# Performance work log

Hardware: AMD Instinct MI355X
Metric: run time of the kernel (lower is better)

## Reference

```python
import jax, jax.numpy as jnp
import numpy as np

D_HID = 512          # RAECell output dim (nn.Linear(1024, 512))
DEPTH = 16           # internal levels -> 2**16 leaves, 131071 nodes


def _levels(left, right, leaf, root):
    """Group internal nodes by depth via host-side BFS (tree topology is static)."""
    levels = []
    frontier = [int(root)]
    while frontier:
        internal = [n for n in frontier if not leaf[n]]
        if internal:
            levels.append(np.asarray(internal, dtype=np.int32))
        frontier = [c for n in internal for c in (int(left[n]), int(right[n]))]
    return levels


def setup_inputs() -> dict:
    key = jax.random.key(0)
    n_leaves = 2 ** DEPTH
    n_nodes = 2 * n_leaves - 1
    first_leaf = n_leaves - 1
    idx = np.arange(n_nodes)
    # complete binary tree in heap layout
    left = np.where(idx < first_leaf, 2 * idx + 1, 0).astype(np.int64)
    right = np.where(idx < first_leaf, 2 * idx + 2, 0).astype(np.int64)
    is_leaf = (idx >= first_leaf).astype(np.int64)
    k1, k2, k3 = jax.random.split(key, 3)
    inp = jax.random.normal(k1, (n_nodes, D_HID), jnp.float32)
    W = jax.random.normal(k2, (D_HID, 2 * D_HID), jnp.float32) * (1.0 / np.sqrt(2 * D_HID))
    b = jax.random.normal(k3, (D_HID,), jnp.float32) * 0.01
    return {
        "left": jnp.asarray(left),
        "right": jnp.asarray(right),
        "is_leaf": jnp.asarray(is_leaf),
        "inp": inp,
        "root": 0,
        "W": W,
        "b": b,
    }


def reference(left, right, is_leaf, inp, root, W, b):
    # Tree indices are static -> pull to host once and batch the recursion
    # level-by-level (replaces the Python recursion + per-node tiny kernels
    # of the original with log2(N) batched concat+GEMM+tanh steps).
    l = np.asarray(left)
    r = np.asarray(right)
    leaf = np.asarray(is_leaf).astype(bool)
    levels = _levels(l, r, leaf, root)
    H = inp  # [n_nodes, 512]; leaf rows are the inputs, internal rows get overwritten bottom-up
    for lvl in reversed(levels):
        a = H[l[lvl]]              # [m, 512] left children
        c = H[r[lvl]]              # [m, 512] right children
        x = jnp.concatenate([a, c], axis=1)          # [m, 1024] == torch.cat((a, b))
        H = H.at[jnp.asarray(lvl)].set(jnp.tanh(x @ W.T + b))
    return H[int(root)]
```

## Files before the change

### kernel.cpp

```cpp
#include <hip/hip_runtime.h>
#include <hip/hip_fp16.h>

typedef _Float16 half8 __attribute__((ext_vector_type(8)));
typedef float f32x4 __attribute__((ext_vector_type(4)));

#define KDIM 1024
#define NDIM 512

#define GLOAD_LDS16(g, l) __builtin_amdgcn_global_load_lds(                 \
    (const __attribute__((address_space(1))) void*)(g),                     \
    (__attribute__((address_space(3))) void*)(l), 16, 0, 0)

__global__ __launch_bounds__(256, 2)
void rae_level_gemm_h(const _Float16* __restrict__ X, const _Float16* __restrict__ Wh,
                      const float* __restrict__ bias, _Float16* __restrict__ Yh)
{
    __shared__ _Float16 Xs[128 * 64];
    __shared__ _Float16 Ws[128 * 64];

    const int tid  = threadIdx.x;
    const int lane = tid & 63;
    const int wave = tid >> 6;
    const int wm = wave >> 1;
    const int wn = wave & 1;
    const int lrow = lane & 15;
    const int lq   = lane >> 4;

    const int brow = blockIdx.x * 128;
    const int bcol = blockIdx.y * 128;

    const int sr = tid >> 3;
    const int su = (((tid & 7) ^ (sr & 7)) << 3);

    const _Float16* xbase = X  + (size_t)(brow + sr) * KDIM + su;
    const _Float16* wbase = Wh + (size_t)(bcol + sr) * KDIM + su;

    f32x4 acc[4][4] = {};

    for (int k0 = 0; k0 < KDIM; k0 += 64) {
        __syncthreads();
        GLOAD_LDS16(xbase + k0,             Xs + tid * 8);
        GLOAD_LDS16(xbase + k0 + 32 * KDIM, Xs + tid * 8 + 2048);
        GLOAD_LDS16(xbase + k0 + 64 * KDIM, Xs + tid * 8 + 4096);
        GLOAD_LDS16(xbase + k0 + 96 * KDIM, Xs + tid * 8 + 6144);
        GLOAD_LDS16(wbase + k0,             Ws + tid * 8);
        GLOAD_LDS16(wbase + k0 + 32 * KDIM, Ws + tid * 8 + 2048);
        GLOAD_LDS16(wbase + k0 + 64 * KDIM, Ws + tid * 8 + 4096);
        GLOAD_LDS16(wbase + k0 + 96 * KDIM, Ws + tid * 8 + 6144);
        __syncthreads();

        #pragma unroll
        for (int ks = 0; ks < 2; ++ks) {
            half8 af[4], bf[4];
            #pragma unroll
            for (int i = 0; i < 4; ++i) {
                const int R = wm * 64 + i * 16 + lrow;
                const int phys = (ks * 4 + lq) ^ (R & 7);
                af[i] = *(const half8*)&Xs[R * 64 + phys * 8];
            }
            #pragma unroll
            for (int j = 0; j < 4; ++j) {
                const int R = wn * 64 + j * 16 + lrow;
                const int phys = (ks * 4 + lq) ^ (R & 7);
                bf[j] = *(const half8*)&Ws[R * 64 + phys * 8];
            }
            #pragma unroll
            for (int i = 0; i < 4; ++i)
                #pragma unroll
                for (int j = 0; j < 4; ++j)
                    acc[i][j] = __builtin_amdgcn_mfma_f32_16x16x32_f16(af[i], bf[j], acc[i][j], 0, 0, 0);
        }
    }

    #pragma unroll
    for (int j = 0; j < 4; ++j) {
        const int col = bcol + wn * 64 + j * 16 + lrow;
        const float bv = bias[col];
        #pragma unroll
        for (int i = 0; i < 4; ++i) {
            const int rbase = brow + wm * 64 + i * 16 + lq * 4;
            #pragma unroll
            for (int r = 0; r < 4; ++r)
                Yh[(size_t)(rbase + r) * NDIM + col] = (_Float16)tanhf(acc[i][j][r] + bv);
        }
    }
}

__global__ __launch_bounds__(256, 2)
void rae_level15_f32(const float* __restrict__ Xf, const _Float16* __restrict__ Wh,
                     const float* __restrict__ bias, _Float16* __restrict__ Yh)
{
    __shared__ _Float16 Xs[128 * 64];
    __shared__ _Float16 Ws[128 * 64];

    const int tid  = threadIdx.x;
    const int lane = tid & 63;
    const int wave = tid >> 6;
    const int wm = wave >> 1;
    const int wn = wave & 1;
    const int lrow = lane & 15;
    const int lq   = lane >> 4;

    const int brow = blockIdx.x * 128;
    const int bcol = blockIdx.y * 128;

    const int sr = tid >> 3;
    const int su = (((tid & 7) ^ (sr & 7)) << 3);

    const float*    xbase = Xf + (size_t)(brow + sr) * KDIM + su;
    const _Float16* wbase = Wh + (size_t)(bcol + sr) * KDIM + su;

    f32x4 acc[4][4] = {};

    for (int k0 = 0; k0 < KDIM; k0 += 64) {
        __syncthreads();
        GLOAD_LDS16(wbase + k0,             Ws + tid * 8);
        GLOAD_LDS16(wbase + k0 + 32 * KDIM, Ws + tid * 8 + 2048);
        GLOAD_LDS16(wbase + k0 + 64 * KDIM, Ws + tid * 8 + 4096);
        GLOAD_LDS16(wbase + k0 + 96 * KDIM, Ws + tid * 8 + 6144);
        #pragma unroll
        for (int c = 0; c < 4; ++c) {
            const float4* g = (const float4*)(xbase + k0 + (size_t)c * 32 * KDIM);
            const float4 aa = g[0];
            const float4 bb = g[1];
            half8 h;
            h[0] = (_Float16)aa.x; h[1] = (_Float16)aa.y;
            h[2] = (_Float16)aa.z; h[3] = (_Float16)aa.w;
            h[4] = (_Float16)bb.x; h[5] = (_Float16)bb.y;
            h[6] = (_Float16)bb.z; h[7] = (_Float16)bb.w;
            *(half8*)(Xs + tid * 8 + c * 2048) = h;
        }
        __syncthreads();

        #pragma unroll
        for (int ks = 0; ks < 2; ++ks) {
            half8 af[4], bf[4];
            #pragma unroll
            for (int i = 0; i < 4; ++i) {
                const int R = wm * 64 + i * 16 + lrow;
                const int phys = (ks * 4 + lq) ^ (R & 7);
                af[i] = *(const half8*)&Xs[R * 64 + phys * 8];
            }
            #pragma unroll
            for (int j = 0; j < 4; ++j) {
                const int R = wn * 64 + j * 16 + lrow;
                const int phys = (ks * 4 + lq) ^ (R & 7);
                bf[j] = *(const half8*)&Ws[R * 64 + phys * 8];
            }
            #pragma unroll
            for (int i = 0; i < 4; ++i)
                #pragma unroll
                for (int j = 0; j < 4; ++j)
                    acc[i][j] = __builtin_amdgcn_mfma_f32_16x16x32_f16(af[i], bf[j], acc[i][j], 0, 0, 0);
        }
    }

    #pragma unroll
    for (int j = 0; j < 4; ++j) {
        const int col = bcol + wn * 64 + j * 16 + lrow;
        const float bv = bias[col];
        #pragma unroll
        for (int i = 0; i < 4; ++i) {
            const int rbase = brow + wm * 64 + i * 16 + lq * 4;
            #pragma unroll
            for (int r = 0; r < 4; ++r)
                Yh[(size_t)(rbase + r) * NDIM + col] = (_Float16)tanhf(acc[i][j][r] + bv);
        }
    }
}

__device__ __forceinline__ void grid_barrier(unsigned* bar, unsigned nb)
{
    __syncthreads();
    if (threadIdx.x == 0) {
        __threadfence();
        unsigned* cnt = bar;
        unsigned* gen = bar + 32;
        unsigned g = __hip_atomic_load(gen, __ATOMIC_RELAXED, __HIP_MEMORY_SCOPE_AGENT);
        if (__hip_atomic_fetch_add(cnt, 1u, __ATOMIC_ACQ_REL, __HIP_MEMORY_SCOPE_AGENT) == nb - 1u) {
            __hip_atomic_store(cnt, 0u, __ATOMIC_RELAXED, __HIP_MEMORY_SCOPE_AGENT);
            __hip_atomic_store(gen, g + 1u, __ATOMIC_RELEASE, __HIP_MEMORY_SCOPE_AGENT);
        } else {
            while (__hip_atomic_load(gen, __ATOMIC_RELAXED, __HIP_MEMORY_SCOPE_AGENT) == g) {}
        }
        __threadfence();
    }
    __syncthreads();
}

#define TWLD 1032

template<int NF>
__device__ __forceinline__ void tail_level(
    int d, const _Float16* __restrict__ Hh, float* __restrict__ out,
    const float* __restrict__ bias, const _Float16* Ws,
    int col0, int gw, int lrow, int lq, _Float16* __restrict__ Y)
{
    const int m = 1 << d;
    const _Float16* X = Hh + ((size_t)(2 << d) - 1) * NDIM;
    const int rbase0 = gw * (NF * 16);
    if (rbase0 >= m) return;

    f32x4 acc[NF][2] = {};

    #pragma unroll
    for (int ks = 0; ks < 32; ++ks) {
        half8 af[NF], bf[2];
        #pragma unroll
        for (int i = 0; i < NF; ++i)
            af[i] = *(const half8*)(X + (size_t)(rbase0 + i * 16 + lrow) * KDIM + ks * 32 + lq * 8);
        #pragma unroll
        for (int j = 0; j < 2; ++j)
            bf[j] = *(const half8*)(Ws + (j * 16 + lrow) * TWLD + ks * 32 + lq * 8);
        #pragma unroll
        for (int i = 0; i < NF; ++i)
            #pragma unroll
            for (int j = 0; j < 2; ++j)
                acc[i][j] = __builtin_amdgcn_mfma_f32_16x16x32_f16(af[i], bf[j], acc[i][j], 0, 0, 0);
    }

    #pragma unroll
    for (int j = 0; j < 2; ++j) {
        const int col = col0 + j * 16 + lrow;
        const float bv = bias[col];
        #pragma unroll
        for (int i = 0; i < NF; ++i) {
            #pragma unroll
            for (int r = 0; r < 4; ++r) {
                const int row = rbase0 + i * 16 + lq * 4 + r;
                if (row < m) {
                    const float v = tanhf(acc[i][j][r] + bv);
                    if (d == 0) out[col] = v;
                    else Y[(size_t)row * NDIM + col] = (_Float16)v;
                }
            }
        }
    }
}

__global__ __launch_bounds__(512, 2)
void rae_tail(const _Float16* __restrict__ Wh, const float* __restrict__ bias,
              _Float16* __restrict__ Hh, float* __restrict__ out,
              unsigned* __restrict__ bar)
{
    __shared__ _Float16 Ws[32 * TWLD];

    const int tid  = threadIdx.x;
    const int lane = tid & 63;
    const int wave = tid >> 6;
    const int lrow = lane & 15;
    const int lq   = lane >> 4;
    const int strip = blockIdx.x & 15;
    const int rgrp  = blockIdx.x >> 4;
    const int col0  = strip * 32;
    const int gw    = wave * 8 + rgrp;

    {
        const _Float16* g = Wh + (size_t)(col0 + (tid >> 4)) * KDIM + (tid & 15) * 64;
        _Float16* l = Ws + (tid >> 4) * TWLD + (tid & 15) * 64;
        #pragma unroll
        for (int j = 0; j < 8; ++j)
            *(half8*)(l + j * 8) = *(const half8*)(g + j * 8);
    }
    __syncthreads();

    for (int d = 11; d >= 0; --d) {
        _Float16* Y = Hh + ((size_t)(1 << d) - 1) * NDIM;
        if (d == 11)
            tail_level<2>(d, Hh, out, bias, Ws, col0, gw, lrow, lq, Y);
        else
            tail_level<1>(d, Hh, out, bias, Ws, col0, gw, lrow, lq, Y);
        if (d) grid_barrier(bar, 128);
    }
}

__global__ void convert_w(const float* __restrict__ W, _Float16* __restrict__ Wh)
{
    const int i = blockIdx.x * 256 + threadIdx.x;
    const float4 v = ((const float4*)W)[i];
    _Float16 o[4] = {(_Float16)v.x, (_Float16)v.y, (_Float16)v.z, (_Float16)v.w};
    *(float2*)(Wh + (size_t)i * 4) = *(float2*)o;
}

extern "C" void kernel_launch(void* const* d_in, const int* in_sizes, int n_in,
                              void* d_out, int out_size, void* d_ws, size_t ws_size,
                              hipStream_t stream)
{
    const float* inp  = (const float*)d_in[3];
    const float* W    = (const float*)d_in[5];
    const float* bias = (const float*)d_in[6];
    float* out = (float*)d_out;

    _Float16* Wh  = (_Float16*)d_ws;
    unsigned* bar = (unsigned*)((char*)d_ws + (1 << 20));
    _Float16* Hh  = (_Float16*)((char*)d_ws + (2 << 20));

    hipMemsetAsync(bar, 0, 256, stream);
    convert_w<<<512, 256, 0, stream>>>(W, Wh);

    rae_level15_f32<<<dim3(256, 4), 256, 0, stream>>>(
        inp + (size_t)65535 * NDIM, Wh, bias, Hh + (size_t)32767 * NDIM);

    for (int d = 14; d >= 12; --d) {
        const int m = 1 << d;
        const _Float16* Xp = Hh + (size_t)((2 << d) - 1) * NDIM;
        _Float16* Yp = Hh + (size_t)((1 << d) - 1) * NDIM;
        rae_level_gemm_h<<<dim3(m / 128, 4), 256, 0, stream>>>(Xp, Wh, bias, Yp);
    }

    rae_tail<<<128, 512, 0, stream>>>(Wh, bias, Hh, out, bar);
}
```

Before: 637.6 us.

## Replace persistent grid-barrier tail with per-level launches and small 8-block tail

```diff
diff --git a/kernel.cpp b/kernel.cpp
--- a/kernel.cpp
+++ b/kernel.cpp
@@ -169,6 +169,59 @@
     }
 }
 
+#define TWLD 1032
+
+__global__ __launch_bounds__(512, 1)
+void rae_strip_level(const _Float16* __restrict__ X, const _Float16* __restrict__ Wh,
+                     const float* __restrict__ bias, _Float16* __restrict__ Y, int m)
+{
+    __shared__ _Float16 Ws[32 * TWLD];
+
+    const int tid  = threadIdx.x;
+    const int lane = tid & 63;
+    const int wave = tid >> 6;
+    const int lrow = lane & 15;
+    const int lq   = lane >> 4;
+    const int strip = blockIdx.x;
+    const int R     = gridDim.y;
+    const int rgrp  = blockIdx.y;
+    const int col0  = strip * 32;
+    const int gw    = wave * R + rgrp;
+
+    {
+        const _Float16* g = Wh + (size_t)(col0 + (tid >> 4)) * KDIM + (tid & 15) * 64;
+        _Float16* l = Ws + (tid >> 4) * TWLD + (tid & 15) * 64;
+        #pragma unroll
+        for (int j = 0; j < 8; ++j)
+            *(half8*)(l + j * 8) = *(const half8*)(g + j * 8);
+    }
+    __syncthreads();
+
+    const int rbase0 = gw * 16;
+    if (rbase0 >= m) return;
+
+    f32x4 acc[2] = {};
+    #pragma unroll
+    for (int ks = 0; ks < 32; ++ks) {
+        const half8 af  = *(const half8*)(X + (size_t)(rbase0 + lrow) * KDIM + ks * 32 + lq * 8);
+        const half8 bf0 = *(const half8*)(Ws + lrow * TWLD + ks * 32 + lq * 8);
+        const half8 bf1 = *(const half8*)(Ws + (16 + lrow) * TWLD + ks * 32 + lq * 8);
+        acc[0] = __builtin_amdgcn_mfma_f32_16x16x32_f16(af, bf0, acc[0], 0, 0, 0);
+        acc[1] = __builtin_amdgcn_mfma_f32_16x16x32_f16(af, bf1, acc[1], 0, 0, 0);
+    }
+
+    #pragma unroll
+    for (int j = 0; j < 2; ++j) {
+        const int col = col0 + j * 16 + lrow;
+        const float bv = bias[col];
+        #pragma unroll
+        for (int r = 0; r < 4; ++r) {
+            const int row = rbase0 + lq * 4 + r;
+            Y[(size_t)row * NDIM + col] = (_Float16)tanhf(acc[j][r] + bv);
+        }
+    }
+}
+
 __device__ __forceinline__ void grid_barrier(unsigned* bar, unsigned nb)
 {
     __syncthreads();
@@ -188,89 +241,58 @@
     __syncthreads();
 }
 
-#define TWLD 1032
-
-template<int NF>
-__device__ __forceinline__ void tail_level(
-    int d, const _Float16* __restrict__ Hh, float* __restrict__ out,
-    const float* __restrict__ bias, const _Float16* Ws,
-    int col0, int gw, int lrow, int lq, _Float16* __restrict__ Y)
-{
-    const int m = 1 << d;
-    const _Float16* X = Hh + ((size_t)(2 << d) - 1) * NDIM;
-    const int rbase0 = gw * (NF * 16);
-    if (rbase0 >= m) return;
-
-    f32x4 acc[NF][2] = {};
-
-    #pragma unroll
-    for (int ks = 0; ks < 32; ++ks) {
-        half8 af[NF], bf[2];
-        #pragma unroll
-        for (int i = 0; i < NF; ++i)
-            af[i] = *(const half8*)(X + (size_t)(rbase0 + i * 16 + lrow) * KDIM + ks * 32 + lq * 8);
-        #pragma unroll
-        for (int j = 0; j < 2; ++j)
-            bf[j] = *(const half8*)(Ws + (j * 16 + lrow) * TWLD + ks * 32 + lq * 8);
-        #pragma unroll
-        for (int i = 0; i < NF; ++i)
-            #pragma unroll
-            for (int j = 0; j < 2; ++j)
-                acc[i][j] = __builtin_amdgcn_mfma_f32_16x16x32_f16(af[i], bf[j], acc[i][j], 0, 0, 0);
-    }
-
-    #pragma unroll
-    for (int j = 0; j < 2; ++j) {
-        const int col = col0 + j * 16 + lrow;
-        const float bv = bias[col];
-        #pragma unroll
-        for (int i = 0; i < NF; ++i) {
-            #pragma unroll
-            for (int r = 0; r < 4; ++r) {
-                const int row = rbase0 + i * 16 + lq * 4 + r;
-                if (row < m) {
-                    const float v = tanhf(acc[i][j][r] + bv);
-                    if (d == 0) out[col] = v;
-                    else Y[(size_t)row * NDIM + col] = (_Float16)v;
-                }
-            }
-        }
-    }
-}
-
-__global__ __launch_bounds__(512, 2)
-void rae_tail(const _Float16* __restrict__ Wh, const float* __restrict__ bias,
-              _Float16* __restrict__ Hh, float* __restrict__ out,
-              unsigned* __restrict__ bar)
-{
-    __shared__ _Float16 Ws[32 * TWLD];
+__global__ __launch_bounds__(512, 1)
+void rae_tail_lo(const _Float16* __restrict__ Wh, const float* __restrict__ bias,
+                 _Float16* __restrict__ Hh, float* __restrict__ out,
+                 unsigned* __restrict__ bar)
+{
+    __shared__ _Float16 Ws[64 * TWLD];
 
     const int tid  = threadIdx.x;
     const int lane = tid & 63;
     const int wave = tid >> 6;
     const int lrow = lane & 15;
     const int lq   = lane >> 4;
-    const int strip = blockIdx.x & 15;
-    const int rgrp  = blockIdx.x >> 4;
-    const int col0  = strip * 32;
-    const int gw    = wave * 8 + rgrp;
+    const int col0 = blockIdx.x * 64;
+    const int rf   = wave & 1;
+    const int cf   = wave >> 1;
 
     {
-        const _Float16* g = Wh + (size_t)(col0 + (tid >> 4)) * KDIM + (tid & 15) * 64;
-        _Float16* l = Ws + (tid >> 4) * TWLD + (tid & 15) * 64;
-        #pragma unroll
-        for (int j = 0; j < 8; ++j)
+        const _Float16* g = Wh + (size_t)(col0 + (tid >> 3)) * KDIM + (tid & 7) * 128;
+        _Float16* l = Ws + (tid >> 3) * TWLD + (tid & 7) * 128;
+        #pragma unroll
+        for (int j = 0; j < 16; ++j)
             *(half8*)(l + j * 8) = *(const half8*)(g + j * 8);
     }
     __syncthreads();
 
-    for (int d = 11; d >= 0; --d) {
+    const int col = col0 + cf * 16 + lrow;
+    const float bv = bias[col];
+
+    for (int d = 5; d >= 0; --d) {
+        const int m = 1 << d;
+        const _Float16* X = Hh + ((size_t)(2 << d) - 1) * NDIM;
         _Float16* Y = Hh + ((size_t)(1 << d) - 1) * NDIM;
-        if (d == 11)
-            tail_level<2>(d, Hh, out, bias, Ws, col0, gw, lrow, lq, Y);
-        else
-            tail_level<1>(d, Hh, out, bias, Ws, col0, gw, lrow, lq, Y);
-        if (d) grid_barrier(bar, 128);
+
+        if (rf * 16 < m) {
+            f32x4 acc = {};
+            #pragma unroll
+            for (int ks = 0; ks < 32; ++ks) {
+                const half8 af = *(const half8*)(X + (size_t)(rf * 16 + lrow) * KDIM + ks * 32 + lq * 8);
+                const half8 bf = *(const half8*)(Ws + (cf * 16 + lrow) * TWLD + ks * 32 + lq * 8);
+                acc = __builtin_amdgcn_mfma_f32_16x16x32_f16(af, bf, acc, 0, 0, 0);
+            }
+            #pragma unroll
+            for (int r = 0; r < 4; ++r) {
+                const int row = rf * 16 + lq * 4 + r;
+                if (row < m) {
+                    const float v = tanhf(acc[r] + bv);
+                    if (d == 0) out[col] = v;
+                    else Y[(size_t)row * NDIM + col] = (_Float16)v;
+                }
+            }
+        }
+        if (d) grid_barrier(bar, 8);
     }
 }
 
@@ -301,12 +323,20 @@
     rae_level15_f32<<<dim3(256, 4), 256, 0, stream>>>(
         inp + (size_t)65535 * NDIM, Wh, bias, Hh + (size_t)32767 * NDIM);
 
-    for (int d = 14; d >= 12; --d) {
+    for (int d = 14; d >= 11; --d) {
         const int m = 1 << d;
         const _Float16* Xp = Hh + (size_t)((2 << d) - 1) * NDIM;
         _Float16* Yp = Hh + (size_t)((1 << d) - 1) * NDIM;
         rae_level_gemm_h<<<dim3(m / 128, 4), 256, 0, stream>>>(Xp, Wh, bias, Yp);
     }
 
-    rae_tail<<<128, 512, 0, stream>>>(Wh, bias, Hh, out, bar);
-}
+    for (int d = 10; d >= 6; --d) {
+        const int m = 1 << d;
+        const int R = (m >= 128) ? (m / 128) : 1;
+        const _Float16* Xp = Hh + (size_t)((2 << d) - 1) * NDIM;
+        _Float16* Yp = Hh + (size_t)((1 << d) - 1) * NDIM;
+        rae_strip_level<<<dim3(16, R), 512, 0, stream>>>(Xp, Wh, bias, Yp, m);
+    }
+
+    rae_tail_lo<<<8, 512, 0, stream>>>(Wh, bias, Hh, out, bar);
+}
```

Result: faster. 588.7 us (-7.7%).
